# Kernel optimization log

Measured on AMD Instinct MI355X. Metric: run time of the kernel, lower is better.

## Reference

```python
import jax, jax.numpy as jnp
import numpy as np

BATCH, SEQ, DIM = 4, 2048, 1024
HEADS = 16
HD = DIM // HEADS  # 64
BASE = 10000.0


def setup_inputs() -> dict:
    key = jax.random.key(0)
    k1, k2, k3 = jax.random.split(key, 3)
    x = jax.random.normal(k1, (BATCH, SEQ, DIM), dtype=jnp.float32)
    # torch Linear weight is (out,in); we store transposed (in,out) so y = x @ w
    w_qkv = jax.random.normal(k2, (DIM, 3 * DIM), dtype=jnp.float32) * (DIM ** -0.5)
    w_out = jax.random.normal(k3, (DIM, DIM), dtype=jnp.float32) * (DIM ** -0.5)
    return {"x": x, "w_qkv": w_qkv, "w_out": w_out}


def _rope_cos_sin(seq_len: int, head_dim: int):
    inv_freq = 1.0 / (BASE ** (jnp.arange(0, head_dim, 2, dtype=jnp.float32) / head_dim))
    t = jnp.arange(seq_len, dtype=jnp.float32)
    freqs = t[:, None] * inv_freq[None, :]          # (S, HD/2)
    emb = jnp.concatenate([freqs, freqs], axis=-1)  # (S, HD)
    return jnp.cos(emb), jnp.sin(emb)


def _rotate_half(x):
    x1, x2 = jnp.split(x, 2, axis=-1)
    return jnp.concatenate([-x2, x1], axis=-1)


def reference(x, w_qkv, w_out):
    B, S, D = x.shape
    qkv = x @ w_qkv                                  # (B,S,3D)
    q, k, v = jnp.split(qkv, 3, axis=-1)
    # (B,S,D) -> (B,H,S,HD)
    q = q.reshape(B, S, HEADS, HD).transpose(0, 2, 1, 3)
    k = k.reshape(B, S, HEADS, HD).transpose(0, 2, 1, 3)
    v = v.reshape(B, S, HEADS, HD).transpose(0, 2, 1, 3)
    cos, sin = _rope_cos_sin(S, HD)                  # (S,HD), broadcast over B,H
    q = q * cos + _rotate_half(q) * sin
    k = k * cos + _rotate_half(k) * sin
    scale = HD ** -0.5
    scores = jnp.einsum('bhqd,bhkd->bhqk', q, k) * scale  # (B,H,S,S)
    causal = jnp.tril(jnp.ones((S, S), dtype=bool))
    scores = jnp.where(causal, scores, -jnp.inf)
    attn = jax.nn.softmax(scores, axis=-1)
    out = jnp.einsum('bhqk,bhkd->bhqd', attn, v)     # (B,H,S,HD)
    out = out.transpose(0, 2, 1, 3).reshape(B, S, D)
    out = out @ w_out
    return out, k, v
```

## Files before the change

### kernel.cpp

```cpp
#include <hip/hip_runtime.h>
#include <hip/hip_bf16.h>
#include <stdint.h>

#define BATCH 4
#define SEQ 2048
#define DIM 1024
#define HEADS 16
#define HD 64
#define BH (BATCH*HEADS)
#define NQKV (3*DIM)

typedef __attribute__((ext_vector_type(8))) short bf16x8;
typedef __attribute__((ext_vector_type(4))) short bf16x4;
typedef __attribute__((ext_vector_type(4))) float f32x4;
typedef __attribute__((ext_vector_type(16))) float f32x16;
typedef __attribute__((ext_vector_type(4))) unsigned u32x4;

#define MFMA16(a,b,c) __builtin_amdgcn_mfma_f32_16x16x32_bf16(a,b,c,0,0,0)
#define MFMA32(a,b,c) __builtin_amdgcn_mfma_f32_32x32x16_bf16(a,b,c,0,0,0)

#if __has_builtin(__builtin_amdgcn_exp2f)
#define EXP2(x) __builtin_amdgcn_exp2f(x)
#else
#define EXP2(x) exp2f(x)
#endif

__device__ inline short f2bf(float f){
    __hip_bfloat16 h = __float2bfloat16(f);
    return *reinterpret_cast<short*>(&h);
}
__device__ inline float bf2f(short s){
    unsigned u = ((unsigned)(unsigned short)s) << 16;
    float f;
    __builtin_memcpy(&f, &u, 4);
    return f;
}
__device__ inline unsigned cvt_pk_bf16(float lo, float hi){
    unsigned r;
    asm("v_cvt_pk_bf16_f32 %0, %1, %2" : "=v"(r) : "v"(lo), "v"(hi));
    return r;
}
__device__ inline short cv1(float f){
    return (short)(cvt_pk_bf16(f, f) & 0xffffu);
}

__global__ void conv_bf16(const float* __restrict__ in, short* __restrict__ out, int n4){
    int i = blockIdx.x*blockDim.x + threadIdx.x;
    f32x4 v = *(const f32x4*)&in[(size_t)i*4];
    unsigned lo = cvt_pk_bf16(v[0], v[1]);
    unsigned hi = cvt_pk_bf16(v[2], v[3]);
    unsigned out2[2] = {lo, hi};
    __builtin_memcpy(&out[(size_t)i*4], out2, 8);
}

__global__ void transpose_conv(const float* __restrict__ in, short* __restrict__ out, int R, int C){
    __shared__ float tile[32][33];
    int c0 = blockIdx.x*32, r0 = blockIdx.y*32;
    int tx = threadIdx.x, ty = threadIdx.y;
    #pragma unroll
    for (int dy = 0; dy < 32; dy += 8)
        tile[ty+dy][tx] = in[(size_t)(r0+ty+dy)*C + c0+tx];
    __syncthreads();
    #pragma unroll
    for (int dy = 0; dy < 32; dy += 8)
        out[(size_t)(c0+ty+dy)*R + r0+tx] = cv1(tile[tx][ty+dy]);
}

template<int WRITE_BF16>
__global__ __launch_bounds__(256) void gemm_bt(const short* __restrict__ A, const short* __restrict__ Bt,
                        void* __restrict__ Cout, int M, int N, int K)
{
    __shared__ short As[2*128*32];
    __shared__ short Bs[2*128*32];
    const int t = threadIdx.x;
    const int lane = t & 63, wave = t >> 6;
    const int wr = wave >> 1, wc = wave & 1;
    const int nbn = N >> 7;
    const int cpx = gridDim.x >> 3;
    const int swz = (blockIdx.x & 7) * cpx + (blockIdx.x >> 3);
    const int bm = swz / nbn, bn = swz % nbn;
    const int m0 = bm*128, n0 = bn*128;
    const int l15 = lane & 15, lhi = lane >> 4;

    f32x4 acc[4][4];
    #pragma unroll
    for (int i=0;i<4;i++)
        #pragma unroll
        for (int j=0;j<4;j++) acc[i][j] = (f32x4){0.f,0.f,0.f,0.f};

    for (int k0 = 0; k0 < K; k0 += 64) {
        #pragma unroll
        for (int kk = 0; kk < 2; ++kk) {
            #pragma unroll
            for (int it = 0; it < 2; ++it) {
                int base = kk*4096 + (it*256 + wave*64)*8;
                int off  = (it*256 + wave*64 + lane)*8;
                int row = off >> 5, col = off & 31;
                __builtin_amdgcn_global_load_lds(
                    (const __attribute__((address_space(1))) void*)(A + (size_t)(m0+row)*K + k0 + kk*32 + col),
                    (__attribute__((address_space(3))) void*)(As + base), 16, 0, 0);
                __builtin_amdgcn_global_load_lds(
                    (const __attribute__((address_space(1))) void*)(Bt + (size_t)(n0+row)*K + k0 + kk*32 + col),
                    (__attribute__((address_space(3))) void*)(Bs + base), 16, 0, 0);
            }
        }
        __syncthreads();
        #pragma unroll
        for (int kk = 0; kk < 2; ++kk) {
            bf16x8 a[4], b[4];
            #pragma unroll
            for (int i=0;i<4;i++)
                a[i] = *(const bf16x8*)&As[kk*4096 + (wr*64 + i*16 + l15)*32 + lhi*8];
            #pragma unroll
            for (int j=0;j<4;j++)
                b[j] = *(const bf16x8*)&Bs[kk*4096 + (wc*64 + j*16 + l15)*32 + lhi*8];
            #pragma unroll
            for (int i=0;i<4;i++)
                #pragma unroll
                for (int j=0;j<4;j++)
                    acc[i][j] = MFMA16(a[i], b[j], acc[i][j]);
        }
        __syncthreads();
    }

    #pragma unroll
    for (int i=0;i<4;i++)
        #pragma unroll
        for (int j=0;j<4;j++)
            #pragma unroll
            for (int jj=0;jj<4;jj++) {
                int row = m0 + wr*64 + i*16 + lhi*4 + jj;
                int col = n0 + wc*64 + j*16 + l15;
                if (WRITE_BF16)
                    ((short*)Cout)[(size_t)row*N + col] = cv1(acc[i][j][jj]);
                else
                    ((float*)Cout)[(size_t)row*N + col] = acc[i][j][jj];
            }
}

__global__ __launch_bounds__(256) void rope_scatter(const short* __restrict__ qkvb,
                             short* __restrict__ qp, short* __restrict__ kp,
                             short* __restrict__ vp,
                             float* __restrict__ kout, float* __restrict__ vout)
{
    __shared__ short vt[64*72];
    const int t = threadIdx.x;
    const int bh = blockIdx.x >> 5;
    const int sb = blockIdx.x & 31;
    const int b = bh >> 4, h = bh & 15;
    const int s_loc = t >> 2, ic = (t & 3) << 3;
    const int s = (sb << 6) + s_loc;
    const size_t rowbase = ((size_t)(b*SEQ + s))*NQKV + h*HD;

    bf16x8 q1 = *(const bf16x8*)&qkvb[rowbase + ic];
    bf16x8 q2 = *(const bf16x8*)&qkvb[rowbase + ic + 32];
    bf16x8 k1 = *(const bf16x8*)&qkvb[rowbase + DIM + ic];
    bf16x8 k2 = *(const bf16x8*)&qkvb[rowbase + DIM + ic + 32];
    bf16x8 v1 = *(const bf16x8*)&qkvb[rowbase + 2*DIM + ic];
    bf16x8 v2 = *(const bf16x8*)&qkvb[rowbase + 2*DIM + ic + 32];

    const float QS = 0.125f * 1.4426950408889634f;
    float q1s[8], q2s[8], k1f[8], k2f[8], v1f[8], v2f[8];
    #pragma unroll
    for (int j=0;j<8;j++){
        int i = ic + j;
        float inv = exp2f(-(float)i * (13.287712379549449f/32.0f));
        float ang = (float)s * inv;
        float sn, cs;
        sincosf(ang, &sn, &cs);
        float q1f = bf2f(q1[j]), q2f = bf2f(q2[j]);
        float ka = bf2f(k1[j]), kb_ = bf2f(k2[j]);
        float qr1 = q1f*cs - q2f*sn, qr2 = q2f*cs + q1f*sn;
        float kr1 = ka*cs - kb_*sn,  kr2 = kb_*cs + ka*sn;
        q1s[j] = qr1*QS; q2s[j] = qr2*QS;
        k1f[j] = kr1; k2f[j] = kr2;
        v1f[j] = bf2f(v1[j]); v2f[j] = bf2f(v2[j]);
    }
    bf16x8 qo1, qo2, ko1, ko2;
    {
        unsigned w[4];
        #pragma unroll
        for (int j=0;j<4;j++) w[j] = cvt_pk_bf16(q1s[2*j], q1s[2*j+1]);
        __builtin_memcpy(&qo1, w, 16);
        #pragma unroll
        for (int j=0;j<4;j++) w[j] = cvt_pk_bf16(q2s[2*j], q2s[2*j+1]);
        __builtin_memcpy(&qo2, w, 16);
        #pragma unroll
        for (int j=0;j<4;j++) w[j] = cvt_pk_bf16(k1f[2*j], k1f[2*j+1]);
        __builtin_memcpy(&ko1, w, 16);
        #pragma unroll
        for (int j=0;j<4;j++) w[j] = cvt_pk_bf16(k2f[2*j], k2f[2*j+1]);
        __builtin_memcpy(&ko2, w, 16);
    }

    const size_t obase = ((size_t)bh*SEQ + s)*HD;
    #pragma unroll
    for (int j4=0;j4<2;j4++){
        *(f32x4*)&kout[obase+ic+j4*4]    = (f32x4){k1f[j4*4],k1f[j4*4+1],k1f[j4*4+2],k1f[j4*4+3]};
        *(f32x4*)&kout[obase+ic+32+j4*4] = (f32x4){k2f[j4*4],k2f[j4*4+1],k2f[j4*4+2],k2f[j4*4+3]};
        *(f32x4*)&vout[obase+ic+j4*4]    = (f32x4){v1f[j4*4],v1f[j4*4+1],v1f[j4*4+2],v1f[j4*4+3]};
        *(f32x4*)&vout[obase+ic+32+j4*4] = (f32x4){v2f[j4*4],v2f[j4*4+1],v2f[j4*4+2],v2f[j4*4+3]};
    }

    {
        const int tkv = (sb << 1) + (s_loc >> 5);
        const int rlo = s_loc & 31;
        const int g1 = ic >> 3,   i1 = g1 >> 1, H1 = g1 & 1;
        const int g2 = 4+(ic>>3), i2 = g2 >> 1, H2 = g2 & 1;
        const size_t tb = ((size_t)bh*64 + tkv)*4;
        *(bf16x8*)&qp[(tb + i1)*512 + (H1*32 + rlo)*8] = qo1;
        *(bf16x8*)&qp[(tb + i2)*512 + (H2*32 + rlo)*8] = qo2;
        *(bf16x8*)&kp[(tb + i1)*512 + (H1*32 + rlo)*8] = ko1;
        *(bf16x8*)&kp[(tb + i2)*512 + (H2*32 + rlo)*8] = ko2;
    }

    #pragma unroll
    for (int j=0;j<8;j++){
        int i = ic + j;
        vt[i*72 + ((((s_loc>>3) ^ (i&7) ^ (i>>3)) & 7)<<3) + (s_loc&7)] = v1[j];
        int i2 = i + 32;
        vt[i2*72 + ((((s_loc>>3) ^ (i2&7) ^ (i2>>3)) & 7)<<3) + (s_loc&7)] = v2[j];
    }
    __syncthreads();

    const int i_out = t >> 2, g = t & 3;
    const int nn = i_out >> 5, l31v = i_out & 31;
    #pragma unroll
    for (int cc=0; cc<2; ++cc){
        int c = 2*g + cc;
        bf16x8 rv = *(const bf16x8*)&vt[i_out*72 + ((((c) ^ (i_out&7) ^ (i_out>>3)) & 7)<<3)];
        int tkv = (sb << 1) + (c >> 2);
        int m = (c >> 1) & 1, H = c & 1;
        size_t va = ((((size_t)bh*64 + tkv)*2 + nn)*2 + m)*512 + (H*32 + l31v)*8;
        *(bf16x8*)&vp[va] = rv;
    }
}

#define ATT_BODY(KU, KP) do { \
    const unsigned sOff = (unsigned)step << 11; \
    { int npos = step + 1; npos = (npos < hi) ? npos : step; \
      const unsigned pOff = (unsigned)npos << 11; \
      _Pragma("unroll") \
      for (int i=0;i<4;i++) \
          KP[i] = *(const bf16x8*)&kbase[pOff + i*512 + lane*8]; } \
    bf16x8 vf[2][2]; \
    _Pragma("unroll") \
    for (int nn=0;nn<2;nn++) \
        _Pragma("unroll") \
        for (int m=0;m<2;m++) \
            vf[nn][m] = *(const bf16x8*)&vbase[sOff + nn*1024 + m*512 + lane*8]; \
    __builtin_amdgcn_s_setprio(1); \
    f32x16 sacc; \
    _Pragma("unroll") \
    for (int rr=0;rr<16;rr++) sacc[rr] = 0.f; \
    _Pragma("unroll") \
    for (int i=0;i<4;i++) \
        sacc = MFMA32(KU[i], qf[i], sacc); \
    __builtin_amdgcn_s_setprio(0); \
    if (step == n-1) { \
        const int kv0 = step << 5; \
        _Pragma("unroll") \
        for (int rr=0;rr<16;rr++){ \
            int kv = kv0 + (rr&3) + 8*(rr>>2) + 4*H; \
            if (kv > q0 + l31) sacc[rr] = -3.0e38f; \
        } \
    } \
    float p[16]; \
    _Pragma("unroll") \
    for (int rr=0;rr<16;rr++) p[rr] = EXP2(sacc[rr]); \
    unsigned W0 = cvt_pk_bf16(p[0],  p[1]); \
    unsigned W1 = cvt_pk_bf16(p[2],  p[3]); \
    unsigned W2 = cvt_pk_bf16(p[4],  p[5]); \
    unsigned W3 = cvt_pk_bf16(p[6],  p[7]); \
    unsigned W4 = cvt_pk_bf16(p[8],  p[9]); \
    unsigned W5 = cvt_pk_bf16(p[10], p[11]); \
    unsigned W6 = cvt_pk_bf16(p[12], p[13]); \
    unsigned W7 = cvt_pk_bf16(p[14], p[15]); \
    asm("v_permlane32_swap_b32 %0, %1" : "+v"(W0), "+v"(W2)); \
    asm("v_permlane32_swap_b32 %0, %1" : "+v"(W1), "+v"(W3)); \
    asm("v_permlane32_swap_b32 %0, %1" : "+v"(W4), "+v"(W6)); \
    asm("v_permlane32_swap_b32 %0, %1" : "+v"(W5), "+v"(W7)); \
    u32x4 paw0 = (u32x4){W0, W1, W2, W3}; \
    u32x4 paw1 = (u32x4){W4, W5, W6, W7}; \
    bf16x8 pa[2]; \
    __builtin_memcpy(&pa[0], &paw0, 16); \
    __builtin_memcpy(&pa[1], &paw1, 16); \
    __builtin_amdgcn_s_setprio(1); \
    _Pragma("unroll") \
    for (int nn=0;nn<2;nn++) \
        _Pragma("unroll") \
        for (int m=0;m<2;m++) \
            o[nn] = MFMA32(pa[m], vf[nn][m], o[nn]); \
    psum = MFMA32(pa[0], onesf, psum); \
    psum = MFMA32(pa[1], onesf, psum); \
    __builtin_amdgcn_s_setprio(0); \
} while(0)

__global__ __launch_bounds__(64) void attn_partial(
        const short* __restrict__ qp, const short* __restrict__ kp,
        const short* __restrict__ vp, short* __restrict__ obuf,
        float* __restrict__ lbuf)
{
    const int lane = threadIdx.x;
    const int wg = blockIdx.x;
    const int x = wg & 7;
    const int r = wg >> 3;
    const int half = r & 1;
    const int pp = (r >> 1) & 31;
    const int bh = (x << 3) | (r >> 6);
    const int l31 = lane & 31;
    const int H = lane >> 5;
    const short* kbase = kp + (size_t)bh * 64 * 2048;
    const short* vbase = vp + (size_t)bh * 64 * 2048;
    const short* qbase = qp + (size_t)bh * 64 * 2048;

    bf16x8 onesf;
    #pragma unroll
    for (int j=0;j<8;j++) onesf[j] = (short)0x3F80;

    #pragma unroll 1
    for (int part = 0; part < 2; ++part) {
        const int qt = part ? (63 - pp) : pp;
        const int q0 = qt << 5;
        const int n  = qt + 1;
        const int mid = (n + 1) >> 1;
        const int lo = half ? mid : 0;
        const int hi = half ? n : mid;

        bf16x8 qf[4];
        #pragma unroll
        for (int i=0;i<4;i++)
            qf[i] = *(const bf16x8*)&qbase[(unsigned)qt*2048 + i*512 + lane*8];

        f32x16 o[2], psum;
        #pragma unroll
        for (int nn=0;nn<2;nn++)
            #pragma unroll
            for (int rr=0;rr<16;rr++) o[nn][rr] = 0.f;
        #pragma unroll
        for (int rr=0;rr<16;rr++) psum[rr] = 0.f;

        if (lo < hi) {
            bf16x8 kfA[4], kfB[4];
            #pragma unroll
            for (int i=0;i<4;i++)
                kfA[i] = *(const bf16x8*)&kbase[(unsigned)lo*2048 + i*512 + lane*8];

            int step = lo;
            while (1) {
                ATT_BODY(kfA, kfB);
                ++step; if (step >= hi) break;
                ATT_BODY(kfB, kfA);
                ++step; if (step >= hi) break;
            }
        }

        short* ob = obuf + (size_t)(((bh << 6) | qt)*2 + half) * 2048;
        #pragma unroll
        for (int nn=0;nn<2;nn++)
            #pragma unroll
            for (int rr=0;rr<16;rr++){
                int qloc = (rr&3) + 8*(rr>>2) + 4*H;
                ob[qloc*64 + nn*32 + l31] = cv1(o[nn][rr]);
            }
        float* lb = lbuf + (size_t)(((bh << 6) | qt)*2 + half) * 32;
        if (l31 == 0) {
            #pragma unroll
            for (int rr=0;rr<16;rr++){
                int qloc = (rr&3) + 8*(rr>>2) + 4*H;
                lb[qloc] = psum[rr];
            }
        }
    }
}
#undef ATT_BODY

__global__ __launch_bounds__(256) void attn_combine(const short* __restrict__ obuf,
                                                    const float* __restrict__ lbuf,
                                                    short* __restrict__ aob)
{
    const int t = threadIdx.x;
    const int tile = blockIdx.x;
    const int bh = tile >> 6, qt = tile & 63;
    const int b = bh >> 4, h = bh & 15;
    const int q0 = qt << 5;
    const short* o0 = obuf + (size_t)(tile*2) * 2048;
    const short* o1 = o0 + 2048;
    const float* lb = lbuf + (size_t)(tile*2) * 32;
    const int row = t >> 3, c0 = (t & 7) << 3;

    float inv = 1.0f / (lb[row] + lb[32 + row]);
    bf16x8 a = *(const bf16x8*)&o0[row*64 + c0];
    bf16x8 bq = *(const bf16x8*)&o1[row*64 + c0];
    float f[8];
    #pragma unroll
    for (int j=0;j<8;j++)
        f[j] = (bf2f(a[j]) + bf2f(bq[j])) * inv;
    unsigned w[4];
    #pragma unroll
    for (int j=0;j<4;j++) w[j] = cvt_pk_bf16(f[2*j], f[2*j+1]);
    bf16x8 ov;
    __builtin_memcpy(&ov, w, 16);
    *(bf16x8*)&aob[((size_t)(b*SEQ + q0 + row))*DIM + h*HD + c0] = ov;
}

extern "C" void kernel_launch(void* const* d_in, const int* in_sizes, int n_in,
                              void* d_out, int out_size, void* d_ws, size_t ws_size,
                              hipStream_t stream) {
    const float* x     = (const float*)d_in[0];
    const float* w_qkv = (const float*)d_in[1];
    const float* w_out = (const float*)d_in[2];
    float* out  = (float*)d_out;
    float* kout = out + (size_t)BATCH*SEQ*DIM;
    float* vout = kout + (size_t)BH*SEQ*HD;

    char* ws = (char*)d_ws;
    short* xb    = (short*)(ws + 0);
    short* wqkvT = (short*)(ws + 16777216);
    short* woutT = (short*)(ws + 23068672);
    short* qkvb  = (short*)(ws + 25165824);
    short* obuf  = (short*)(ws + 25165824);
    float* lbuf  = (float*)(ws + 25165824 + 33554432);
    short* qp    = (short*)(ws + 75497472);
    short* kp    = (short*)(ws + 92274688);
    short* vp    = (short*)(ws + 109051904);
    short* aob   = (short*)(ws + 125829120);

    conv_bf16<<<(BATCH*SEQ*DIM)/1024, 256, 0, stream>>>(x, xb, (BATCH*SEQ*DIM)/4);
    transpose_conv<<<dim3(NQKV/32, DIM/32), dim3(32,8), 0, stream>>>(w_qkv, wqkvT, DIM, NQKV);
    transpose_conv<<<dim3(DIM/32, DIM/32), dim3(32,8), 0, stream>>>(w_out, woutT, DIM, DIM);

    gemm_bt<1><<<(8192/128)*(NQKV/128), 256, 0, stream>>>(xb, wqkvT, qkvb, 8192, NQKV, DIM);

    rope_scatter<<<BH*(SEQ/64), 256, 0, stream>>>(qkvb, qp, kp, vp, kout, vout);

    attn_partial<<<4096, 64, 0, stream>>>(qp, kp, vp, obuf, lbuf);
    attn_combine<<<4096, 256, 0, stream>>>(obuf, lbuf, aob);

    gemm_bt<0><<<(8192/128)*(DIM/128), 256, 0, stream>>>(aob, woutT, out, 8192, DIM, DIM);
}
```

Before: 208.2 us.

## Fuse RoPE and Q/K/V scatter into QKV GEMM epilogue

Replaces the QKV GEMM plus separate rope_scatter kernel with one GEMM whose epilogue applies RoPE and the Q scale in registers. It writes fp32 k/v outputs directly and packs the bf16 q/k/v tiles into the attention layouts through a swizzled LDS staging buffer. This removes the intermediate qkvb buffer's write and re-read and one kernel launch. In exchange the epilogue is heavier, with sincos per element, uncoalesced strided fp32 stores, and scalar LDS gathers for the V transpose.

Result: slower. 255.0 us (+22.5%).

```diff
diff --git a/kernel.cpp b/kernel.cpp
--- a/kernel.cpp
+++ b/kernel.cpp
@@ -11,7 +11,6 @@
 #define NQKV (3*DIM)
 
 typedef __attribute__((ext_vector_type(8))) short bf16x8;
-typedef __attribute__((ext_vector_type(4))) short bf16x4;
 typedef __attribute__((ext_vector_type(4))) float f32x4;
 typedef __attribute__((ext_vector_type(16))) float f32x16;
 typedef __attribute__((ext_vector_type(4))) unsigned u32x4;
@@ -25,10 +24,6 @@
 #define EXP2(x) exp2f(x)
 #endif
 
-__device__ inline short f2bf(float f){
-    __hip_bfloat16 h = __float2bfloat16(f);
-    return *reinterpret_cast<short*>(&h);
-}
 __device__ inline float bf2f(short s){
     unsigned u = ((unsigned)(unsigned short)s) << 16;
     float f;
@@ -138,101 +133,148 @@
             }
 }
 
-__global__ __launch_bounds__(256) void rope_scatter(const short* __restrict__ qkvb,
-                             short* __restrict__ qp, short* __restrict__ kp,
-                             short* __restrict__ vp,
-                             float* __restrict__ kout, float* __restrict__ vout)
+__global__ __launch_bounds__(256) void gemm_qkv(const short* __restrict__ A, const short* __restrict__ Bt,
+        short* __restrict__ qp, short* __restrict__ kp, short* __restrict__ vp,
+        float* __restrict__ kout, float* __restrict__ vout)
 {
-    __shared__ short vt[64*72];
+    __shared__ short smem[16384];
+    short* As = smem;
+    short* Bs = smem + 8192;
+    const int K = 1024;
     const int t = threadIdx.x;
-    const int bh = blockIdx.x >> 5;
-    const int sb = blockIdx.x & 31;
-    const int b = bh >> 4, h = bh & 15;
-    const int s_loc = t >> 2, ic = (t & 3) << 3;
-    const int s = (sb << 6) + s_loc;
-    const size_t rowbase = ((size_t)(b*SEQ + s))*NQKV + h*HD;
-
-    bf16x8 q1 = *(const bf16x8*)&qkvb[rowbase + ic];
-    bf16x8 q2 = *(const bf16x8*)&qkvb[rowbase + ic + 32];
-    bf16x8 k1 = *(const bf16x8*)&qkvb[rowbase + DIM + ic];
-    bf16x8 k2 = *(const bf16x8*)&qkvb[rowbase + DIM + ic + 32];
-    bf16x8 v1 = *(const bf16x8*)&qkvb[rowbase + 2*DIM + ic];
-    bf16x8 v2 = *(const bf16x8*)&qkvb[rowbase + 2*DIM + ic + 32];
-
-    const float QS = 0.125f * 1.4426950408889634f;
-    float q1s[8], q2s[8], k1f[8], k2f[8], v1f[8], v2f[8];
-    #pragma unroll
-    for (int j=0;j<8;j++){
-        int i = ic + j;
-        float inv = exp2f(-(float)i * (13.287712379549449f/32.0f));
-        float ang = (float)s * inv;
-        float sn, cs;
-        sincosf(ang, &sn, &cs);
-        float q1f = bf2f(q1[j]), q2f = bf2f(q2[j]);
-        float ka = bf2f(k1[j]), kb_ = bf2f(k2[j]);
-        float qr1 = q1f*cs - q2f*sn, qr2 = q2f*cs + q1f*sn;
-        float kr1 = ka*cs - kb_*sn,  kr2 = kb_*cs + ka*sn;
-        q1s[j] = qr1*QS; q2s[j] = qr2*QS;
-        k1f[j] = kr1; k2f[j] = kr2;
-        v1f[j] = bf2f(v1[j]); v2f[j] = bf2f(v2[j]);
-    }
-    bf16x8 qo1, qo2, ko1, ko2;
-    {
-        unsigned w[4];
-        #pragma unroll
-        for (int j=0;j<4;j++) w[j] = cvt_pk_bf16(q1s[2*j], q1s[2*j+1]);
-        __builtin_memcpy(&qo1, w, 16);
-        #pragma unroll
-        for (int j=0;j<4;j++) w[j] = cvt_pk_bf16(q2s[2*j], q2s[2*j+1]);
-        __builtin_memcpy(&qo2, w, 16);
-        #pragma unroll
-        for (int j=0;j<4;j++) w[j] = cvt_pk_bf16(k1f[2*j], k1f[2*j+1]);
-        __builtin_memcpy(&ko1, w, 16);
-        #pragma unroll
-        for (int j=0;j<4;j++) w[j] = cvt_pk_bf16(k2f[2*j], k2f[2*j+1]);
-        __builtin_memcpy(&ko2, w, 16);
-    }
-
-    const size_t obase = ((size_t)bh*SEQ + s)*HD;
-    #pragma unroll
-    for (int j4=0;j4<2;j4++){
-        *(f32x4*)&kout[obase+ic+j4*4]    = (f32x4){k1f[j4*4],k1f[j4*4+1],k1f[j4*4+2],k1f[j4*4+3]};
-        *(f32x4*)&kout[obase+ic+32+j4*4] = (f32x4){k2f[j4*4],k2f[j4*4+1],k2f[j4*4+2],k2f[j4*4+3]};
-        *(f32x4*)&vout[obase+ic+j4*4]    = (f32x4){v1f[j4*4],v1f[j4*4+1],v1f[j4*4+2],v1f[j4*4+3]};
-        *(f32x4*)&vout[obase+ic+32+j4*4] = (f32x4){v2f[j4*4],v2f[j4*4+1],v2f[j4*4+2],v2f[j4*4+3]};
-    }
-
-    {
-        const int tkv = (sb << 1) + (s_loc >> 5);
-        const int rlo = s_loc & 31;
-        const int g1 = ic >> 3,   i1 = g1 >> 1, H1 = g1 & 1;
-        const int g2 = 4+(ic>>3), i2 = g2 >> 1, H2 = g2 & 1;
-        const size_t tb = ((size_t)bh*64 + tkv)*4;
-        *(bf16x8*)&qp[(tb + i1)*512 + (H1*32 + rlo)*8] = qo1;
-        *(bf16x8*)&qp[(tb + i2)*512 + (H2*32 + rlo)*8] = qo2;
-        *(bf16x8*)&kp[(tb + i1)*512 + (H1*32 + rlo)*8] = ko1;
-        *(bf16x8*)&kp[(tb + i2)*512 + (H2*32 + rlo)*8] = ko2;
-    }
-
-    #pragma unroll
-    for (int j=0;j<8;j++){
-        int i = ic + j;
-        vt[i*72 + ((((s_loc>>3) ^ (i&7) ^ (i>>3)) & 7)<<3) + (s_loc&7)] = v1[j];
-        int i2 = i + 32;
-        vt[i2*72 + ((((s_loc>>3) ^ (i2&7) ^ (i2>>3)) & 7)<<3) + (s_loc&7)] = v2[j];
-    }
+    const int lane = t & 63, wave = t >> 6;
+    const int wr = wave >> 1, wc = wave & 1;
+    const int l31 = lane & 31, H = lane >> 5;
+    const int nbn = 24;
+    const int cpx = gridDim.x >> 3;
+    const int swz = (blockIdx.x & 7) * cpx + (blockIdx.x >> 3);
+    const int bm = swz / nbn, bn = swz % nbn;
+    const int m0 = bm*128, n0 = bn*128;
+    const int l15 = lane & 15, lhi = lane >> 4;
+
+    f32x4 acc[4][4];
+    #pragma unroll
+    for (int i=0;i<4;i++)
+        #pragma unroll
+        for (int j=0;j<4;j++) acc[i][j] = (f32x4){0.f,0.f,0.f,0.f};
+
+    for (int k0 = 0; k0 < K; k0 += 64) {
+        #pragma unroll
+        for (int kk = 0; kk < 2; ++kk) {
+            #pragma unroll
+            for (int it = 0; it < 2; ++it) {
+                int base = kk*4096 + (it*256 + wave*64)*8;
+                int off  = (it*256 + wave*64 + lane)*8;
+                int row = off >> 5, col = off & 31;
+                __builtin_amdgcn_global_load_lds(
+                    (const __attribute__((address_space(1))) void*)(A + (size_t)(m0+row)*K + k0 + kk*32 + col),
+                    (__attribute__((address_space(3))) void*)(As + base), 16, 0, 0);
+                __builtin_amdgcn_global_load_lds(
+                    (const __attribute__((address_space(1))) void*)(Bt + (size_t)(n0+row)*K + k0 + kk*32 + col),
+                    (__attribute__((address_space(3))) void*)(Bs + base), 16, 0, 0);
+            }
+        }
+        __syncthreads();
+        #pragma unroll
+        for (int kk = 0; kk < 2; ++kk) {
+            bf16x8 a[4], b[4];
+            #pragma unroll
+            for (int i=0;i<4;i++)
+                a[i] = *(const bf16x8*)&As[kk*4096 + (wr*64 + i*16 + l15)*32 + lhi*8];
+            #pragma unroll
+            for (int j=0;j<4;j++)
+                b[j] = *(const bf16x8*)&Bs[kk*4096 + (wc*64 + j*16 + l15)*32 + lhi*8];
+            #pragma unroll
+            for (int i=0;i<4;i++)
+                #pragma unroll
+                for (int j=0;j<4;j++)
+                    acc[i][j] = MFMA16(a[i], b[j], acc[i][j]);
+        }
+        __syncthreads();
+    }
+
+    const int third = bn >> 3;
+    const int h2 = (bn & 7) << 1;
+    const int b = bm >> 4;
+    const int s0 = (bm & 15) << 7;
+
+    if (third < 2) {
+        const float QSs = (third == 0) ? (0.125f * 1.4426950408889634f) : 1.0f;
+        #pragma unroll
+        for (int j=0;j<2;j++){
+            float inv = exp2f(-(float)(j*16 + l15) * (13.287712379549449f/32.0f));
+            #pragma unroll
+            for (int i=0;i<4;i++){
+                #pragma unroll
+                for (int jj=0;jj<4;jj++){
+                    float ang = (float)(s0 + wr*64 + i*16 + lhi*4 + jj) * inv;
+                    float sn, cs;
+                    sincosf(ang, &sn, &cs);
+                    float x1 = acc[i][j][jj], x2 = acc[i][j+2][jj];
+                    acc[i][j][jj]   = (x1*cs - x2*sn) * QSs;
+                    acc[i][j+2][jj] = (x2*cs + x1*sn) * QSs;
+                }
+            }
+        }
+    }
+
+    if (third >= 1) {
+        float* fout = (third == 1) ? kout : vout;
+        #pragma unroll
+        for (int i=0;i<4;i++)
+            #pragma unroll
+            for (int j=0;j<4;j++){
+                int h = h2 + wc;
+                int ihd = j*16 + l15;
+                size_t base = (((size_t)(b*16 + h)*SEQ) + (s0 + wr*64 + i*16 + lhi*4)) * HD + ihd;
+                #pragma unroll
+                for (int jj=0;jj<4;jj++)
+                    fout[base + (size_t)jj*HD] = acc[i][j][jj];
+            }
+    }
+
+    short* Cs = smem;
+    #pragma unroll
+    for (int i=0;i<4;i++)
+        #pragma unroll
+        for (int j=0;j<4;j++)
+            #pragma unroll
+            for (int jj=0;jj<4;jj++){
+                int row = wr*64 + i*16 + lhi*4 + jj;
+                int cb  = ((wc*64 + j*16 + l15) * 2) ^ ((row & 7) << 4);
+                *(short*)((char*)Cs + row*256 + cb) = cv1(acc[i][j][jj]);
+            }
     __syncthreads();
 
-    const int i_out = t >> 2, g = t & 3;
-    const int nn = i_out >> 5, l31v = i_out & 31;
-    #pragma unroll
-    for (int cc=0; cc<2; ++cc){
-        int c = 2*g + cc;
-        bf16x8 rv = *(const bf16x8*)&vt[i_out*72 + ((((c) ^ (i_out&7) ^ (i_out>>3)) & 7)<<3)];
-        int tkv = (sb << 1) + (c >> 2);
-        int m = (c >> 1) & 1, H = c & 1;
-        size_t va = ((((size_t)bh*64 + tkv)*2 + nn)*2 + m)*512 + (H*32 + l31v)*8;
-        *(bf16x8*)&vp[va] = rv;
+    if (third < 2) {
+        short* dst = (third == 0) ? qp : kp;
+        #pragma unroll
+        for (int u=0;u<8;u++){
+            int g = wave*8 + u;
+            int i2 = g & 3, head = (g>>2)&1, t4 = g>>3;
+            int row = t4*32 + l31;
+            int cb = ((head*64 + i2*16 + H*8)*2) ^ ((row & 7) << 4);
+            bf16x8 v = *(const bf16x8*)((const char*)Cs + row*256 + cb);
+            size_t base = (((size_t)(b*16 + h2 + head)*64) + (s0>>5) + t4) * 2048 + i2*512;
+            *(bf16x8*)&dst[base + lane*8] = v;
+        }
+    } else {
+        #pragma unroll
+        for (int u=0;u<8;u++){
+            int g = wave*8 + u;
+            int m_ = g & 1, nn = (g>>1)&1, head = (g>>2)&1, t4 = g>>3;
+            short tmp[8];
+            #pragma unroll
+            for (int j=0;j<8;j++){
+                int row = t4*32 + m_*16 + H*8 + j;
+                int cb = ((head*64 + nn*32 + l31)*2) ^ ((row & 7) << 4);
+                tmp[j] = *(const short*)((const char*)Cs + row*256 + cb);
+            }
+            bf16x8 v;
+            __builtin_memcpy(&v, tmp, 16);
+            size_t base = ((((size_t)(b*16 + h2 + head)*64 + (s0>>5) + t4)*2 + nn)*2 + m_) * 512;
+            *(bf16x8*)&vp[base + lane*8] = v;
+        }
     }
 }
 
@@ -418,7 +460,6 @@
     short* xb    = (short*)(ws + 0);
     short* wqkvT = (short*)(ws + 16777216);
     short* woutT = (short*)(ws + 23068672);
-    short* qkvb  = (short*)(ws + 25165824);
     short* obuf  = (short*)(ws + 25165824);
     float* lbuf  = (float*)(ws + 25165824 + 33554432);
     short* qp    = (short*)(ws + 75497472);
@@ -430,9 +471,7 @@
     transpose_conv<<<dim3(NQKV/32, DIM/32), dim3(32,8), 0, stream>>>(w_qkv, wqkvT, DIM, NQKV);
     transpose_conv<<<dim3(DIM/32, DIM/32), dim3(32,8), 0, stream>>>(w_out, woutT, DIM, DIM);
 
-    gemm_bt<1><<<(8192/128)*(NQKV/128), 256, 0, stream>>>(xb, wqkvT, qkvb, 8192, NQKV, DIM);
-
-    rope_scatter<<<BH*(SEQ/64), 256, 0, stream>>>(qkvb, qp, kp, vp, kout, vout);
+    gemm_qkv<<<(8192/128)*(NQKV/128), 256, 0, stream>>>(xb, wqkvT, qp, kp, vp, kout, vout);
 
     attn_partial<<<4096, 64, 0, stream>>>(qp, kp, vp, obuf, lbuf);
     attn_combine<<<4096, 256, 0, stream>>>(obuf, lbuf, aob);
```

## Double-buffer GEMM LDS tiles to overlap the next K-slice load with MFMAs

Applied to the files above, without the earlier changes.

Restructures the bf16 GEMM main loop into a double-buffered pipeline. The first 32-wide K slice is loaded up front. Each iteration then issues direct-to-LDS global loads for the next slice into the other buffer before running the MFMAs on the current one, with a single barrier per step. This aims to hide global-load latency behind matrix math that was previously serialized, and it raises wave priority around the MFMA block. In exchange the K-step per iteration is halved, so barriers and loop overhead double, and the gain depends on the barrier's vmcnt wait not draining the prefetch too early.

Measured after the change: 212.4 us. +2.0%, slower.

```diff
diff --git a/kernel.cpp b/kernel.cpp
--- a/kernel.cpp
+++ b/kernel.cpp
@@ -70,8 +70,8 @@
 __global__ __launch_bounds__(256) void gemm_bt(const short* __restrict__ A, const short* __restrict__ Bt,
                         void* __restrict__ Cout, int M, int N, int K)
 {
-    __shared__ short As[2*128*32];
-    __shared__ short Bs[2*128*32];
+    __shared__ short As[2][128*32];
+    __shared__ short Bs[2][128*32];
     const int t = threadIdx.x;
     const int lane = t & 63, wave = t >> 6;
     const int wr = wave >> 1, wc = wave & 1;
@@ -82,45 +82,69 @@
     const int m0 = bm*128, n0 = bn*128;
     const int l15 = lane & 15, lhi = lane >> 4;
 
+    const int base0 = (wave*64)*8;
+    const int base1 = (256 + wave*64)*8;
+    const int off0  = base0 + lane*8;
+    const int off1  = base1 + lane*8;
+    const int row0 = off0 >> 5, col0 = off0 & 31;
+    const int row1 = off1 >> 5, col1 = off1 & 31;
+
     f32x4 acc[4][4];
     #pragma unroll
     for (int i=0;i<4;i++)
         #pragma unroll
         for (int j=0;j<4;j++) acc[i][j] = (f32x4){0.f,0.f,0.f,0.f};
 
-    for (int k0 = 0; k0 < K; k0 += 64) {
-        #pragma unroll
-        for (int kk = 0; kk < 2; ++kk) {
-            #pragma unroll
-            for (int it = 0; it < 2; ++it) {
-                int base = kk*4096 + (it*256 + wave*64)*8;
-                int off  = (it*256 + wave*64 + lane)*8;
-                int row = off >> 5, col = off & 31;
-                __builtin_amdgcn_global_load_lds(
-                    (const __attribute__((address_space(1))) void*)(A + (size_t)(m0+row)*K + k0 + kk*32 + col),
-                    (__attribute__((address_space(3))) void*)(As + base), 16, 0, 0);
-                __builtin_amdgcn_global_load_lds(
-                    (const __attribute__((address_space(1))) void*)(Bt + (size_t)(n0+row)*K + k0 + kk*32 + col),
-                    (__attribute__((address_space(3))) void*)(Bs + base), 16, 0, 0);
-            }
+    {
+        __builtin_amdgcn_global_load_lds(
+            (const __attribute__((address_space(1))) void*)(A + (size_t)(m0+row0)*K + col0),
+            (__attribute__((address_space(3))) void*)(&As[0][base0]), 16, 0, 0);
+        __builtin_amdgcn_global_load_lds(
+            (const __attribute__((address_space(1))) void*)(Bt + (size_t)(n0+row0)*K + col0),
+            (__attribute__((address_space(3))) void*)(&Bs[0][base0]), 16, 0, 0);
+        __builtin_amdgcn_global_load_lds(
+            (const __attribute__((address_space(1))) void*)(A + (size_t)(m0+row1)*K + col1),
+            (__attribute__((address_space(3))) void*)(&As[0][base1]), 16, 0, 0);
+        __builtin_amdgcn_global_load_lds(
+            (const __attribute__((address_space(1))) void*)(Bt + (size_t)(n0+row1)*K + col1),
+            (__attribute__((address_space(3))) void*)(&Bs[0][base1]), 16, 0, 0);
+    }
+    __syncthreads();
+
+    int cur = 0;
+    for (int k0 = 0; k0 < K; k0 += 32) {
+        if (k0 + 32 < K) {
+            const int kn = k0 + 32;
+            const int nb = cur ^ 1;
+            __builtin_amdgcn_global_load_lds(
+                (const __attribute__((address_space(1))) void*)(A + (size_t)(m0+row0)*K + kn + col0),
+                (__attribute__((address_space(3))) void*)(&As[nb][base0]), 16, 0, 0);
+            __builtin_amdgcn_global_load_lds(
+                (const __attribute__((address_space(1))) void*)(Bt + (size_t)(n0+row0)*K + kn + col0),
+                (__attribute__((address_space(3))) void*)(&Bs[nb][base0]), 16, 0, 0);
+            __builtin_amdgcn_global_load_lds(
+                (const __attribute__((address_space(1))) void*)(A + (size_t)(m0+row1)*K + kn + col1),
+                (__attribute__((address_space(3))) void*)(&As[nb][base1]), 16, 0, 0);
+            __builtin_amdgcn_global_load_lds(
+                (const __attribute__((address_space(1))) void*)(Bt + (size_t)(n0+row1)*K + kn + col1),
+                (__attribute__((address_space(3))) void*)(&Bs[nb][base1]), 16, 0, 0);
         }
+        bf16x8 a[4], b[4];
+        #pragma unroll
+        for (int i=0;i<4;i++)
+            a[i] = *(const bf16x8*)&As[cur][(wr*64 + i*16 + l15)*32 + lhi*8];
+        #pragma unroll
+        for (int j=0;j<4;j++)
+            b[j] = *(const bf16x8*)&Bs[cur][(wc*64 + j*16 + l15)*32 + lhi*8];
+        __builtin_amdgcn_s_setprio(1);
+        #pragma unroll
+        for (int i=0;i<4;i++)
+            #pragma unroll
+            for (int j=0;j<4;j++)
+                acc[i][j] = MFMA16(a[i], b[j], acc[i][j]);
+        __builtin_amdgcn_s_setprio(0);
         __syncthreads();
-        #pragma unroll
-        for (int kk = 0; kk < 2; ++kk) {
-            bf16x8 a[4], b[4];
-            #pragma unroll
-            for (int i=0;i<4;i++)
-                a[i] = *(const bf16x8*)&As[kk*4096 + (wr*64 + i*16 + l15)*32 + lhi*8];
-            #pragma unroll
-            for (int j=0;j<4;j++)
-                b[j] = *(const bf16x8*)&Bs[kk*4096 + (wc*64 + j*16 + l15)*32 + lhi*8];
-            #pragma unroll
-            for (int i=0;i<4;i++)
-                #pragma unroll
-                for (int j=0;j<4;j++)
-                    acc[i][j] = MFMA16(a[i], b[j], acc[i][j]);
-        }
-        __syncthreads();
+        cur ^= 1;
     }
 
     #pragma unroll
```
